# Optimization experiments

Measured on AMD Instinct MI355X. Metric: run time of the kernel, lower is better.

The kernel has to match this reference:

```python
import jax, jax.numpy as jnp
import numpy as np

EPSILON = 1e-7  # wl-coref utils.add_dummy epsilon
LEAKY_SLOPE = 0.01  # torch.nn.LeakyReLU default

N_MENTIONS = 10000
BATCH = 512
N_ANTS = 50
MENTION_EMB = 1024
PW_EMB = 64
IN_FEATURES = 3 * MENTION_EMB + PW_EMB  # 3136
HIDDEN = 128


def setup_inputs() -> dict:
    key = jax.random.key(0)
    ks = jax.random.split(key, 9)
    return {
        "all_mentions": jax.random.normal(ks[0], (N_MENTIONS, MENTION_EMB), jnp.float32),
        "mentions_batch": jax.random.normal(ks[1], (BATCH, MENTION_EMB), jnp.float32),
        "pw_batch": jax.random.normal(ks[2], (BATCH, N_ANTS, PW_EMB), jnp.float32),
        "top_indices_batch": jax.random.randint(ks[3], (BATCH, N_ANTS), 0, N_MENTIONS, jnp.int64 if jax.config.jax_enable_x64 else jnp.int32),
        "top_rough_scores_batch": jax.random.normal(ks[4], (BATCH, N_ANTS), jnp.float32),
        "W1": jax.random.normal(ks[5], (IN_FEATURES, HIDDEN), jnp.float32) * 0.02,
        "b1": jax.random.normal(ks[6], (HIDDEN,), jnp.float32) * 0.02,
        "W_out": jax.random.normal(ks[7], (HIDDEN, 1), jnp.float32) * 0.02,
        "b_out": jax.random.normal(ks[8], (1,), jnp.float32) * 0.02,
    }


def reference(all_mentions, mentions_batch, pw_batch, top_indices_batch,
              top_rough_scores_batch, W1, b1, W_out, b_out):
    batch, n_ants = top_indices_batch.shape
    emb = mentions_batch.shape[1]
    # pair matrix: [batch, n_ants, 3*emb + pw_emb]
    a_mentions = jnp.broadcast_to(mentions_batch[:, None, :], (batch, n_ants, emb))
    b_mentions = all_mentions[top_indices_batch]          # gather: [batch, n_ants, emb]
    similarity = a_mentions * b_mentions
    pair_matrix = jnp.concatenate((a_mentions, b_mentions, similarity, pw_batch), axis=2)
    # FFNN: Linear -> LeakyReLU -> (Dropout=identity in eval) -> Linear(out=1)
    h = jax.nn.leaky_relu(jnp.einsum('baf,fh->bah', pair_matrix, W1) + b1, LEAKY_SLOPE)
    ffnn = (jnp.einsum('bah,ho->bao', h, W_out) + b_out)[..., 0]  # [batch, n_ants]
    scores = top_rough_scores_batch + ffnn
    # add_dummy(eps=True): prepend a column of EPSILON
    dummy = jnp.full((batch, 1), EPSILON, dtype=scores.dtype)
    return jnp.concatenate((dummy, scores), axis=1)  # [batch, n_ants + 1]
```

## Files before the change

kernel.cpp:

```cpp
#include <hip/hip_runtime.h>

#define N_MENT   10000
#define BATCH    512
#define N_ANTS   50
#define EMB      1024
#define PW_EMB   64
#define IN_F     3136
#define HID      128
#define M_TOT    (BATCH * N_ANTS)
#define EPS_VAL  1e-7f
#define SLOPE    0.01f

#define NKT      98
#define CONV_BLK 196
#define MAIN_BLK BATCH

using f32x4 = __attribute__((ext_vector_type(4))) float;
using s16x8 = __attribute__((ext_vector_type(8))) short;
using u16x4 = __attribute__((ext_vector_type(4))) unsigned short;
using u16x8 = __attribute__((ext_vector_type(8))) unsigned short;

__device__ __forceinline__ unsigned short f2bf(float f) {
  unsigned u = __builtin_bit_cast(unsigned, f);
  u += 0x7FFFu + ((u >> 16) & 1u);
  return (unsigned short)(u >> 16);
}

__device__ __forceinline__ u16x4 pack4(float4 v) {
  union { u16x4 o; unsigned u[2]; } r;
  asm("v_cvt_pk_bf16_f32 %0, %1, %2" : "=v"(r.u[0]) : "v"(v.x), "v"(v.y));
  asm("v_cvt_pk_bf16_f32 %0, %1, %2" : "=v"(r.u[1]) : "v"(v.z), "v"(v.w));
  return r.o;
}

__device__ __forceinline__ float4 fmul4(float4 a, float4 b) {
  return make_float4(a.x * b.x, a.y * b.y, a.z * b.z, a.w * b.w);
}

__device__ __forceinline__ int tile_orig_k(int tk) {
  if (tk >= 96) return 3072 + (tk - 96) * 32;
  const int c = tk / 6, r = tk % 6;
  return (r >> 1) * 1024 + c * 64 + (r & 1) * 32;
}

__global__ __launch_bounds__(256) void k_convert(const float* __restrict__ w1,
                                                 unsigned short* __restrict__ w1f) {
  const int id   = blockIdx.x * 256 + threadIdx.x;
  const int lane = id & 63;
  const int tile = id >> 6;
  const int tk   = tile % NKT, tn = tile / NKT;
  const int n    = tn * 16 + (lane & 15);
  const int k    = tile_orig_k(tk) + (lane >> 4) * 8;
  u16x8 o;
  #pragma unroll
  for (int j = 0; j < 8; ++j) o[j] = f2bf(w1[(size_t)(k + j) * HID + n]);
  *(u16x8*)(w1f + (size_t)id * 8) = o;
}

__global__ __launch_bounds__(512) void k_main(
    const float* __restrict__ all_m, const float* __restrict__ men,
    const float* __restrict__ pw, const int* __restrict__ topi,
    const float* __restrict__ rough, const unsigned short* __restrict__ w1f,
    const float* __restrict__ b1, const float* __restrict__ wout,
    const float* __restrict__ bout, float* __restrict__ out) {
  __shared__ __align__(16) unsigned short Xs[2][3][64 * 72];
  __shared__ float red[8][64];

  const int t   = threadIdx.x;
  const int bid = blockIdx.x;
  const int mbase = bid * N_ANTS;

  const int sr = t >> 3, sq = t & 7;
  const int r  = sr < N_ANTS ? sr : N_ANTS - 1;
  const int m  = mbase + r;
  const int bidx = topi[m];
  const float* pA = men   + (size_t)bid  * EMB    + sq * 8;
  const float* pB = all_m + (size_t)bidx * EMB    + sq * 8;
  const float* pP = pw    + (size_t)m    * PW_EMB + sq * 8;

  const int lane = t & 63, wid = t >> 6;
  const int ln = lane & 15, lg = lane >> 4;
  const unsigned short* wf = w1f + (size_t)wid * NKT * 512 + lane * 8;

  f32x4 acc[4] = {};

  float4 av0 = ((const float4*)pA)[0], av1 = ((const float4*)pA)[1];
  float4 bv0 = ((const float4*)pB)[0], bv1 = ((const float4*)pB)[1];

  s16x8 wcur[6], wnext[6];
  #pragma unroll
  for (int j = 0; j < 6; ++j)
    wcur[j] = *(const s16x8*)(wf + (size_t)j * 512);

  int buf = 0;
  for (int c = 0; c < 16; ++c) {
    *(u16x4*)&Xs[buf][0][sr * 72 + sq * 8]     = pack4(av0);
    *(u16x4*)&Xs[buf][0][sr * 72 + sq * 8 + 4] = pack4(av1);
    *(u16x4*)&Xs[buf][1][sr * 72 + sq * 8]     = pack4(bv0);
    *(u16x4*)&Xs[buf][1][sr * 72 + sq * 8 + 4] = pack4(bv1);
    *(u16x4*)&Xs[buf][2][sr * 72 + sq * 8]     = pack4(fmul4(av0, bv0));
    *(u16x4*)&Xs[buf][2][sr * 72 + sq * 8 + 4] = pack4(fmul4(av1, bv1));

    if (c < 15) {
      const float* qA = pA + (c + 1) * 64;
      const float* qB = pB + (c + 1) * 64;
      av0 = ((const float4*)qA)[0]; av1 = ((const float4*)qA)[1];
      bv0 = ((const float4*)qB)[0]; bv1 = ((const float4*)qB)[1];
    } else {
      av0 = ((const float4*)pP)[0]; av1 = ((const float4*)pP)[1];
    }

    #pragma unroll
    for (int j = 0; j < 6; ++j) {
      const int tkn = (c < 15) ? (c + 1) * 6 + j : (j < 2 ? 96 + j : 97);
      wnext[j] = *(const s16x8*)(wf + (size_t)tkn * 512);
    }

    __syncthreads();
    #pragma unroll
    for (int j = 0; j < 6; ++j) {
      const int reg = j >> 1, ks = j & 1;
      #pragma unroll
      for (int mt = 0; mt < 4; ++mt) {
        s16x8 x = *(const s16x8*)&Xs[buf][reg][(mt * 16 + ln) * 72 + ks * 32 + lg * 8];
        acc[mt] = __builtin_amdgcn_mfma_f32_16x16x32_bf16(x, wcur[j], acc[mt], 0, 0, 0);
      }
    }
    #pragma unroll
    for (int j = 0; j < 6; ++j) wcur[j] = wnext[j];
    buf ^= 1;
  }

  {
    *(u16x4*)&Xs[buf][0][sr * 72 + sq * 8]     = pack4(av0);
    *(u16x4*)&Xs[buf][0][sr * 72 + sq * 8 + 4] = pack4(av1);
    __syncthreads();
    #pragma unroll
    for (int ks = 0; ks < 2; ++ks)
      #pragma unroll
      for (int mt = 0; mt < 4; ++mt) {
        s16x8 x = *(const s16x8*)&Xs[buf][0][(mt * 16 + ln) * 72 + ks * 32 + lg * 8];
        acc[mt] = __builtin_amdgcn_mfma_f32_16x16x32_bf16(x, wcur[ks], acc[mt], 0, 0, 0);
      }
  }

  const int n0 = wid * 16 + ln;
  const float bias = b1[n0], w_o = wout[n0];
  #pragma unroll
  for (int mt = 0; mt < 4; ++mt)
    #pragma unroll
    for (int e = 0; e < 4; ++e) {
      float h = acc[mt][e] + bias;
      h = h > 0.f ? h : SLOPE * h;
      float ss = h * w_o;
      ss += __shfl_xor(ss, 1);
      ss += __shfl_xor(ss, 2);
      ss += __shfl_xor(ss, 4);
      ss += __shfl_xor(ss, 8);
      if (ln == 0) red[wid][mt * 16 + lg * 4 + e] = ss;
    }
  __syncthreads();
  if (t < N_ANTS) {
    const int gm = mbase + t;
    float v = red[0][t];
    #pragma unroll
    for (int w = 1; w < 8; ++w) v += red[w][t];
    out[(size_t)bid * (N_ANTS + 1) + 1 + t] = rough[gm] + v + bout[0];
  }
  if (t == 0) out[(size_t)bid * (N_ANTS + 1)] = EPS_VAL;
}

__global__ void k_eps(float* __restrict__ out) {
  out[(size_t)threadIdx.x * (N_ANTS + 1)] = EPS_VAL;
}

__global__ __launch_bounds__(128) void k_fb(const float* __restrict__ all_m,
                                            const float* __restrict__ men,
                                            const float* __restrict__ pw,
                                            const int*   __restrict__ topi,
                                            const float* __restrict__ rough,
                                            const float* __restrict__ w1,
                                            const float* __restrict__ b1,
                                            const float* __restrict__ wout,
                                            const float* __restrict__ bout,
                                            float* __restrict__ out) {
  __shared__ float xs[IN_F];
  __shared__ float hred[HID];
  const int pair = blockIdx.x;
  const int t = threadIdx.x;
  const int bb = pair / N_ANTS;
  const int idx = topi[pair];
  const float* pA = men + (size_t)bb * EMB;
  const float* pB = all_m + (size_t)idx * EMB;
  for (int k = t; k < EMB; k += 128) {
    float a = pA[k], b = pB[k];
    xs[k] = a; xs[EMB + k] = b; xs[2 * EMB + k] = a * b;
  }
  if (t < PW_EMB) xs[3 * EMB + t] = pw[(size_t)pair * PW_EMB + t];
  __syncthreads();
  float acc = 0.f;
  for (int k = 0; k < IN_F; ++k) acc = fmaf(xs[k], w1[(size_t)k * HID + t], acc);
  acc += b1[t];
  acc = acc > 0.f ? acc : SLOPE * acc;
  hred[t] = acc * wout[t];
  __syncthreads();
  for (int off = 64; off > 0; off >>= 1) {
    if (t < off) hred[t] += hred[t + off];
    __syncthreads();
  }
  if (t == 0)
    out[(size_t)bb * (N_ANTS + 1) + 1 + (pair - bb * N_ANTS)] = rough[pair] + hred[0] + bout[0];
}

extern "C" void kernel_launch(void* const* d_in, const int* in_sizes, int n_in,
                              void* d_out, int out_size, void* d_ws, size_t ws_size,
                              hipStream_t stream) {
  const float* all_m = (const float*)d_in[0];
  const float* men   = (const float*)d_in[1];
  const float* pw    = (const float*)d_in[2];
  const int*   topi  = (const int*)  d_in[3];
  const float* rough = (const float*)d_in[4];
  const float* w1    = (const float*)d_in[5];
  const float* b1    = (const float*)d_in[6];
  const float* wout  = (const float*)d_in[7];
  const float* bout  = (const float*)d_in[8];
  float* out = (float*)d_out;

  const size_t W1F_BYTES = (size_t)HID * IN_F * sizeof(unsigned short);

  if (ws_size >= W1F_BYTES) {
    unsigned short* w1f = (unsigned short*)d_ws;
    k_convert<<<CONV_BLK, 256, 0, stream>>>(w1, w1f);
    k_main<<<MAIN_BLK, 512, 0, stream>>>(all_m, men, pw, topi, rough, w1f,
                                         b1, wout, bout, out);
  } else {
    k_eps<<<1, BATCH, 0, stream>>>(out);
    k_fb<<<M_TOT, 128, 0, stream>>>(all_m, men, pw, topi, rough, w1, b1, wout, bout, out);
  }
}
```

Measured before the change: 48.89 us.

## Split each batch row across two blocks and swizzle LDS tile layout

```diff
diff --git a/kernel.cpp b/kernel.cpp
--- a/kernel.cpp
+++ b/kernel.cpp
@@ -13,7 +13,7 @@
 
 #define NKT      98
 #define CONV_BLK 196
-#define MAIN_BLK BATCH
+#define MAIN_BLK (BATCH * 2)
 
 using f32x4 = __attribute__((ext_vector_type(4))) float;
 using s16x8 = __attribute__((ext_vector_type(8))) short;
@@ -63,29 +63,41 @@
     const float* __restrict__ rough, const unsigned short* __restrict__ w1f,
     const float* __restrict__ b1, const float* __restrict__ wout,
     const float* __restrict__ bout, float* __restrict__ out) {
-  __shared__ __align__(16) unsigned short Xs[2][3][64 * 72];
-  __shared__ float red[8][64];
+  __shared__ __align__(16) unsigned short Xs[2][3][32 * 64];
+  __shared__ float red[8][32];
 
   const int t   = threadIdx.x;
   const int bid = blockIdx.x;
-  const int mbase = bid * N_ANTS;
-
-  const int sr = t >> 3, sq = t & 7;
-  const int r  = sr < N_ANTS ? sr : N_ANTS - 1;
+  const int br  = bid >> 1;
+  const int half = bid & 1;
+  const int mbase = br * N_ANTS + half * 25;
+
+  const int sr = t >> 4, sq = t & 15;
+  const int r  = sr < 25 ? sr : 24;
   const int m  = mbase + r;
   const int bidx = topi[m];
-  const float* pA = men   + (size_t)bid  * EMB    + sq * 8;
-  const float* pB = all_m + (size_t)bidx * EMB    + sq * 8;
-  const float* pP = pw    + (size_t)m    * PW_EMB + sq * 8;
+  const float* pA = men   + (size_t)br   * EMB    + sq * 4;
+  const float* pB = all_m + (size_t)bidx * EMB    + sq * 4;
+  const float* pP = pw    + (size_t)m    * PW_EMB + sq * 4;
+  const int widx = sr * 64 + (((sq * 8) ^ ((sr & 7) << 4)) >> 1);
 
   const int lane = t & 63, wid = t >> 6;
   const int ln = lane & 15, lg = lane >> 4;
   const unsigned short* wf = w1f + (size_t)wid * NKT * 512 + lane * 8;
 
-  f32x4 acc[4] = {};
-
-  float4 av0 = ((const float4*)pA)[0], av1 = ((const float4*)pA)[1];
-  float4 bv0 = ((const float4*)pB)[0], bv1 = ((const float4*)pB)[1];
+  int ridx[2][2];
+  #pragma unroll
+  for (int ks = 0; ks < 2; ++ks)
+    #pragma unroll
+    for (int mt = 0; mt < 2; ++mt) {
+      const int R = mt * 16 + ln;
+      ridx[ks][mt] = R * 64 + (((ks * 64 + lg * 16) ^ ((R & 7) << 4)) >> 1);
+    }
+
+  f32x4 acc[2] = {};
+
+  float4 av = ((const float4*)pA)[0];
+  float4 bv = ((const float4*)pB)[0];
 
   s16x8 wcur[6], wnext[6];
   #pragma unroll
@@ -94,20 +106,15 @@
 
   int buf = 0;
   for (int c = 0; c < 16; ++c) {
-    *(u16x4*)&Xs[buf][0][sr * 72 + sq * 8]     = pack4(av0);
-    *(u16x4*)&Xs[buf][0][sr * 72 + sq * 8 + 4] = pack4(av1);
-    *(u16x4*)&Xs[buf][1][sr * 72 + sq * 8]     = pack4(bv0);
-    *(u16x4*)&Xs[buf][1][sr * 72 + sq * 8 + 4] = pack4(bv1);
-    *(u16x4*)&Xs[buf][2][sr * 72 + sq * 8]     = pack4(fmul4(av0, bv0));
-    *(u16x4*)&Xs[buf][2][sr * 72 + sq * 8 + 4] = pack4(fmul4(av1, bv1));
+    *(u16x4*)&Xs[buf][0][widx] = pack4(av);
+    *(u16x4*)&Xs[buf][1][widx] = pack4(bv);
+    *(u16x4*)&Xs[buf][2][widx] = pack4(fmul4(av, bv));
 
     if (c < 15) {
-      const float* qA = pA + (c + 1) * 64;
-      const float* qB = pB + (c + 1) * 64;
-      av0 = ((const float4*)qA)[0]; av1 = ((const float4*)qA)[1];
-      bv0 = ((const float4*)qB)[0]; bv1 = ((const float4*)qB)[1];
+      av = ((const float4*)(pA + (c + 1) * 64))[0];
+      bv = ((const float4*)(pB + (c + 1) * 64))[0];
     } else {
-      av0 = ((const float4*)pP)[0]; av1 = ((const float4*)pP)[1];
+      av = ((const float4*)pP)[0];
     }
 
     #pragma unroll
@@ -121,8 +128,8 @@
     for (int j = 0; j < 6; ++j) {
       const int reg = j >> 1, ks = j & 1;
       #pragma unroll
-      for (int mt = 0; mt < 4; ++mt) {
-        s16x8 x = *(const s16x8*)&Xs[buf][reg][(mt * 16 + ln) * 72 + ks * 32 + lg * 8];
+      for (int mt = 0; mt < 2; ++mt) {
+        s16x8 x = *(const s16x8*)&Xs[buf][reg][ridx[ks][mt]];
         acc[mt] = __builtin_amdgcn_mfma_f32_16x16x32_bf16(x, wcur[j], acc[mt], 0, 0, 0);
       }
     }
@@ -132,14 +139,13 @@
   }
 
   {
-    *(u16x4*)&Xs[buf][0][sr * 72 + sq * 8]     = pack4(av0);
-    *(u16x4*)&Xs[buf][0][sr * 72 + sq * 8 + 4] = pack4(av1);
+    *(u16x4*)&Xs[buf][0][widx] = pack4(av);
     __syncthreads();
     #pragma unroll
     for (int ks = 0; ks < 2; ++ks)
       #pragma unroll
-      for (int mt = 0; mt < 4; ++mt) {
-        s16x8 x = *(const s16x8*)&Xs[buf][0][(mt * 16 + ln) * 72 + ks * 32 + lg * 8];
+      for (int mt = 0; mt < 2; ++mt) {
+        s16x8 x = *(const s16x8*)&Xs[buf][0][ridx[ks][mt]];
         acc[mt] = __builtin_amdgcn_mfma_f32_16x16x32_bf16(x, wcur[ks], acc[mt], 0, 0, 0);
       }
   }
@@ -147,7 +153,7 @@
   const int n0 = wid * 16 + ln;
   const float bias = b1[n0], w_o = wout[n0];
   #pragma unroll
-  for (int mt = 0; mt < 4; ++mt)
+  for (int mt = 0; mt < 2; ++mt)
     #pragma unroll
     for (int e = 0; e < 4; ++e) {
       float h = acc[mt][e] + bias;
@@ -160,14 +166,15 @@
       if (ln == 0) red[wid][mt * 16 + lg * 4 + e] = ss;
     }
   __syncthreads();
-  if (t < N_ANTS) {
+  if (t < 25) {
     const int gm = mbase + t;
     float v = red[0][t];
     #pragma unroll
     for (int w = 1; w < 8; ++w) v += red[w][t];
-    out[(size_t)bid * (N_ANTS + 1) + 1 + t] = rough[gm] + v + bout[0];
-  }
-  if (t == 0) out[(size_t)bid * (N_ANTS + 1)] = EPS_VAL;
+    out[(size_t)br * (N_ANTS + 1) + 1 + half * 25 + t] = rough[gm] + v + bout[0];
+  }
+  if (t == 0 && half == 0)
+    out[(size_t)br * (N_ANTS + 1)] = EPS_VAL;
 }
 
 __global__ void k_eps(float* __restrict__ out) {
```

Result: slower. 54.06 us (+10.6%).
